# Kernel tuning notes

Measured on AMD Instinct MI355X. Metric: run time of the kernel, lower is better.

## Reference

```python
import jax, jax.numpy as jnp
import numpy as np

D_MODEL = 512
N_HEADS = 8
HEAD_SIZE = 64


def setup_inputs() -> dict:
    key = jax.random.key(0)
    ks = jax.random.split(key, 6)
    B, T = 4, 2048
    x_q = jax.random.normal(ks[0], (B, T, D_MODEL), dtype=jnp.float32)
    s = 1.0 / np.sqrt(D_MODEL)
    # per-head q/k/v projection weights, stacked: [H, head_size, d_model]
    Wq = jax.random.normal(ks[1], (N_HEADS, HEAD_SIZE, D_MODEL), dtype=jnp.float32) * s
    Wk = jax.random.normal(ks[2], (N_HEADS, HEAD_SIZE, D_MODEL), dtype=jnp.float32) * s
    Wv = jax.random.normal(ks[3], (N_HEADS, HEAD_SIZE, D_MODEL), dtype=jnp.float32) * s
    Wp = jax.random.normal(ks[4], (D_MODEL, D_MODEL), dtype=jnp.float32) * s
    bp = jax.random.normal(ks[5], (D_MODEL,), dtype=jnp.float32) * 0.01
    return {"x_q": x_q, "Wq": Wq, "Wk": Wk, "Wv": Wv, "Wp": Wp, "bp": bp}


def reference(x_q, Wq, Wk, Wv, Wp, bp):
    B, T, C = x_q.shape  # C == d_model
    # per-head projections: [B, H, T, K]
    q = jnp.einsum('btd,hkd->bhtk', x_q, Wq)
    k = jnp.einsum('btd,hkd->bhtk', x_q, Wk)
    v = jnp.einsum('btd,hkd->bhtk', x_q, Wv)
    # NOTE: original scales by C**-0.5 with C = d_model (not head_size)
    scores = jnp.einsum('bhtk,bhsk->bhts', q, k) * (C ** -0.5)
    causal = jnp.tril(jnp.ones((T, T), dtype=bool))
    scores = jnp.where(causal, scores, -jnp.inf)
    wei = jax.nn.softmax(scores, axis=-1)  # dropout is identity in eval
    out = jnp.einsum('bhts,bhsk->bhtk', wei, v)
    # concat heads: [B, T, H*K] == [B, T, d_model]
    out = out.transpose(0, 2, 1, 3).reshape(B, T, C)
    return out @ Wp.T + bp
```

## Files before the change

kernel.cpp:

```cpp
#include <hip/hip_runtime.h>
#include <hip/hip_bf16.h>

using bf16x8 = __attribute__((ext_vector_type(8))) __bf16;
using f32x4  = __attribute__((ext_vector_type(4))) float;
using f32x16 = __attribute__((ext_vector_type(16))) float;
using i32x4  = __attribute__((ext_vector_type(4))) int;

#define MFMA_16x16x32(a, b, c) __builtin_amdgcn_mfma_f32_16x16x32_bf16((a), (b), (c), 0, 0, 0)
#define MFMA32(a, b, c)        __builtin_amdgcn_mfma_f32_32x32x16_bf16((a), (b), (c), 0, 0, 0)

__device__ __forceinline__ ushort f2bf(float f) {
    return __builtin_bit_cast(ushort, (__bf16)f);
}
__device__ __forceinline__ unsigned pk_bf16(float lo, float hi) {
    unsigned r;
    asm volatile("v_cvt_pk_bf16_f32 %0, %1, %2" : "=v"(r) : "v"(lo), "v"(hi));
    return r;
}
__device__ __forceinline__ void pl32_swap(unsigned &a, unsigned &b) {
    asm volatile("v_permlane32_swap_b32 %0, %1" : "+v"(a), "+v"(b));
}

__global__ __launch_bounds__(256) void cvt_bf16(
    const float* __restrict__ in, ushort* __restrict__ out, int n)
{
    const int i = (blockIdx.x * 256 + threadIdx.x) * 8;
    if (i + 8 <= n) {
        const f32x4 a = *(const f32x4*)(in + i);
        const f32x4 b = *(const f32x4*)(in + i + 4);
        union { ushort u[8]; i32x4 w; } p;
        #pragma unroll
        for (int j = 0; j < 4; ++j) { p.u[j] = f2bf(a[j]); p.u[4 + j] = f2bf(b[j]); }
        *(i32x4*)(out + i) = p.w;
    }
}

__global__ __launch_bounds__(256) void cvt_w3(
    const float* __restrict__ w0, const float* __restrict__ w1,
    const float* __restrict__ w2, ushort* __restrict__ out)
{
    const int i = (blockIdx.x * 256 + threadIdx.x) * 8;
    const int w = i >> 18, off = i & 262143;
    const float* src = (w == 0) ? w0 : ((w == 1) ? w1 : w2);
    const f32x4 a = *(const f32x4*)(src + off);
    const f32x4 b = *(const f32x4*)(src + off + 4);
    union { ushort u[8]; i32x4 v; } p;
    #pragma unroll
    for (int j = 0; j < 4; ++j) { p.u[j] = f2bf(a[j]); p.u[4 + j] = f2bf(b[j]); }
    *(i32x4*)(out + i) = p.v;
}

__global__ __launch_bounds__(256) void gemm_qkv3(
    const ushort* __restrict__ A, const ushort* __restrict__ Wbf,
    float qscale, ushort* __restrict__ qb, ushort* __restrict__ kb,
    ushort* __restrict__ vb)
{
    __shared__ ushort lA[128][40];
    __shared__ ushort lB[128][40];
    const int wsel = blockIdx.y >> 2;
    const int n0 = (blockIdx.y & 3) * 128;
    const ushort* W = Wbf + wsel * 262144;
    ushort* out = (wsel == 0) ? qb : ((wsel == 1) ? kb : vb);
    const float scale = (wsel == 0) ? qscale : 1.0f;

    const int m0 = blockIdx.x * 128;
    const int tid  = threadIdx.x;
    const int lane = tid & 63;
    const int wave = tid >> 6;
    const int wr = (wave >> 1) * 64, wc = (wave & 1) * 64;
    const int frow = lane & 15, fk = (lane >> 4) * 8;
    const int sr = tid >> 1, scc = (tid & 1) * 16;

    f32x4 acc[4][4] = {};
    i32x4 va0, va1, vb0, vb1;
    auto load = [&](int k0) {
        const ushort* pa = A + (m0 + sr) * 512 + k0 + scc;
        va0 = *(const i32x4*)(pa);
        va1 = *(const i32x4*)(pa + 8);
        const ushort* pb = W + (n0 + sr) * 512 + k0 + scc;
        vb0 = *(const i32x4*)(pb);
        vb1 = *(const i32x4*)(pb + 8);
    };

    load(0);
    for (int t = 0; t < 16; ++t) {
        __syncthreads();
        *(i32x4*)&lA[sr][scc]     = va0;
        *(i32x4*)&lA[sr][scc + 8] = va1;
        *(i32x4*)&lB[sr][scc]     = vb0;
        *(i32x4*)&lB[sr][scc + 8] = vb1;
        if (t + 1 < 16) load((t + 1) * 32);
        __syncthreads();

        bf16x8 af[4], bg[4];
        #pragma unroll
        for (int m = 0; m < 4; ++m) af[m] = *(const bf16x8*)&lA[wr + m * 16 + frow][fk];
        #pragma unroll
        for (int n = 0; n < 4; ++n) bg[n] = *(const bf16x8*)&lB[wc + n * 16 + frow][fk];
        #pragma unroll
        for (int m = 0; m < 4; ++m)
            #pragma unroll
            for (int n = 0; n < 4; ++n)
                acc[m][n] = MFMA_16x16x32(af[m], bg[n], acc[m][n]);
    }

    const int rbase = (lane >> 4) * 4;
    const int ccol  = lane & 15;
    if (wsel == 2) {
        #pragma unroll
        for (int m = 0; m < 4; ++m)
            #pragma unroll
            for (int n = 0; n < 4; ++n) {
                const int col = n0 + wc + n * 16 + ccol;
                const int row0 = m0 + wr + m * 16 + rbase;
                unsigned long long u = 0;
                #pragma unroll
                for (int r = 0; r < 4; ++r)
                    u |= ((unsigned long long)f2bf(acc[m][n][r])) << (16 * r);
                const size_t idx = ((size_t)((row0 >> 11) * 8 + (col >> 6)) * 64
                                    + (col & 63)) * 2048 + (row0 & 2047);
                *(unsigned long long*)(out + idx) = u;
            }
    } else {
        #pragma unroll
        for (int m = 0; m < 4; ++m)
            #pragma unroll
            for (int n = 0; n < 4; ++n) {
                const int col = n0 + wc + n * 16 + ccol;
                #pragma unroll
                for (int r = 0; r < 4; ++r) {
                    const int row = m0 + wr + m * 16 + rbase + r;
                    out[(((row >> 11) * 8 + (col >> 6)) * 2048 + (row & 2047)) * 64 + (col & 63)]
                        = f2bf(acc[m][n][r] * scale);
                }
            }
    }
}

__global__ __launch_bounds__(256) void gemm_out(
    const ushort* __restrict__ A, const float* __restrict__ W,
    const float* __restrict__ bias, float* __restrict__ out)
{
    __shared__ ushort lA[128][40];
    __shared__ ushort lB[128][40];
    const int m0 = blockIdx.x * 128;
    const int n0 = blockIdx.y * 128;
    const int tid  = threadIdx.x;
    const int lane = tid & 63;
    const int wave = tid >> 6;
    const int wr = (wave >> 1) * 64, wc = (wave & 1) * 64;
    const int frow = lane & 15, fk = (lane >> 4) * 8;
    const int sr = tid >> 1, scc = (tid & 1) * 16;

    f32x4 acc[4][4] = {};
    i32x4 va0, va1;
    f32x4 b0, b1, b2, b3;
    auto load = [&](int k0) {
        const int row = m0 + sr, c = k0 + scc;
        const ushort* pa = A + ((((row >> 11) * 8 + (c >> 6)) * 2048 + (row & 2047)) * 64 + (c & 63));
        va0 = *(const i32x4*)(pa);
        va1 = *(const i32x4*)(pa + 8);
        const float* pb = W + (n0 + sr) * 512 + k0 + scc;
        b0 = *(const f32x4*)(pb);
        b1 = *(const f32x4*)(pb + 4);
        b2 = *(const f32x4*)(pb + 8);
        b3 = *(const f32x4*)(pb + 12);
    };

    load(0);
    for (int t = 0; t < 16; ++t) {
        union { ushort u[16]; i32x4 w[2]; } pB;
        #pragma unroll
        for (int j = 0; j < 4; ++j) {
            pB.u[j]      = f2bf(b0[j]);  pB.u[4 + j]  = f2bf(b1[j]);
            pB.u[8 + j]  = f2bf(b2[j]);  pB.u[12 + j] = f2bf(b3[j]);
        }
        __syncthreads();
        *(i32x4*)&lA[sr][scc]     = va0;
        *(i32x4*)&lA[sr][scc + 8] = va1;
        *(i32x4*)&lB[sr][scc]     = pB.w[0];
        *(i32x4*)&lB[sr][scc + 8] = pB.w[1];
        if (t + 1 < 16) load((t + 1) * 32);
        __syncthreads();

        bf16x8 af[4], bg[4];
        #pragma unroll
        for (int m = 0; m < 4; ++m) af[m] = *(const bf16x8*)&lA[wr + m * 16 + frow][fk];
        #pragma unroll
        for (int n = 0; n < 4; ++n) bg[n] = *(const bf16x8*)&lB[wc + n * 16 + frow][fk];
        #pragma unroll
        for (int m = 0; m < 4; ++m)
            #pragma unroll
            for (int n = 0; n < 4; ++n)
                acc[m][n] = MFMA_16x16x32(af[m], bg[n], acc[m][n]);
    }

    const int rbase = (lane >> 4) * 4;
    const int ccol  = lane & 15;
    #pragma unroll
    for (int m = 0; m < 4; ++m)
        #pragma unroll
        for (int n = 0; n < 4; ++n) {
            const int col = n0 + wc + n * 16 + ccol;
            const float bv = bias[col];
            #pragma unroll
            for (int r = 0; r < 4; ++r) {
                const int row = m0 + wr + m * 16 + rbase + r;
                out[row * 512 + col] = acc[m][n][r] + bv;
            }
        }
}

__global__ __launch_bounds__(256, 2) void attn_kernel(
    const ushort* __restrict__ q, const ushort* __restrict__ k,
    const ushort* __restrict__ vt, ushort* __restrict__ att)
{
    __shared__ ushort lK[2][64][64];
    __shared__ ushort lV[2][64][64];

    const int NB   = (int)(gridDim.x * gridDim.y);
    const int NH   = NB >> 4;
    const int half = NB >> 1;
    const int n    = (int)(blockIdx.y * gridDim.x + blockIdx.x);
    const int r    = (n < half) ? n : (NB - 1 - (n - half));
    const int qt0  = (15 - r / NH) * 128;
    const int bh   = r % NH;

    const ushort* Q  = q  + (size_t)bh * 2048 * 64;
    const ushort* K  = k  + (size_t)bh * 2048 * 64;
    const ushort* VT = vt + (size_t)bh * 2048 * 64;
    ushort* O = att + (size_t)bh * 2048 * 64;

    const int tid = threadIdx.x;
    const int wv  = tid >> 6;
    const int l   = tid & 63;
    const int ql  = l & 31;
    const int hi  = l >> 5;
    const int wrow0 = qt0 + wv * 32;
    const int qrow  = wrow0 + ql;
    const int wmax  = wrow0 + 31;
    const int qkey  = ql & 7;
    const float LOG2E = 1.44269504088896f;

    const int srow = tid >> 2;
    const int sg   = (tid & 3) * 2;
    const int skey = srow & 7;

    bf16x8 aq[4];
    #pragma unroll
    for (int kk = 0; kk < 4; ++kk)
        aq[kk] = *(const bf16x8*)(Q + (size_t)qrow * 64 + kk * 16 + hi * 8);

    f32x16 o0 = {}, o1 = {};
    float mrun = -30000.0f, lrun = 0.0f;
    const int nt = qt0 / 64 + 2;

    i32x4 kr0, kr1, vr0, vr1;
    auto loadG = [&](int s0) {
        const ushort* kp = K + (size_t)(s0 + srow) * 64 + (tid & 3) * 16;
        kr0 = *(const i32x4*)(kp);
        kr1 = *(const i32x4*)(kp + 8);
        const ushort* vp = VT + (size_t)srow * 2048 + s0 + (tid & 3) * 16;
        vr0 = *(const i32x4*)(vp);
        vr1 = *(const i32x4*)(vp + 8);
    };
    auto writeL = [&](int b) {
        *(i32x4*)&lK[b][srow][((sg    ) ^ skey) * 8] = kr0;
        *(i32x4*)&lK[b][srow][((sg + 1) ^ skey) * 8] = kr1;
        *(i32x4*)&lV[b][srow][((sg    ) ^ skey) * 8] = vr0;
        *(i32x4*)&lV[b][srow][((sg + 1) ^ skey) * 8] = vr1;
    };

    loadG(0);
    writeL(0);
    if (nt > 1) loadG(64);

    for (int t = 0; t < nt; ++t) {
        const int p  = t & 1;
        const int s0 = t * 64;
        __syncthreads();
        if (t + 1 < nt) writeL(p ^ 1);
        if (t + 2 < nt) loadG(s0 + 128);

        if (s0 > wmax) continue;

        f32x16 sa = {}, sb = {};
        #pragma unroll
        for (int kk = 0; kk < 4; ++kk) {
            const bf16x8 kb0 = *(const bf16x8*)&lK[p][ql]     [((2 * kk + hi) ^ qkey) * 8];
            const bf16x8 kb1 = *(const bf16x8*)&lK[p][32 + ql][((2 * kk + hi) ^ qkey) * 8];
            sa = MFMA32(kb0, aq[kk], sa);
            sb = MFMA32(kb1, aq[kk], sb);
        }

        if (s0 + 63 > wrow0) {
            #pragma unroll
            for (int rr = 0; rr < 16; ++rr) {
                const int cr = (rr & 3) + 8 * (rr >> 2) + 4 * hi;
                if (s0 + cr > qrow)      sa[rr] = -30000.0f;
                if (s0 + 32 + cr > qrow) sb[rr] = -30000.0f;
            }
        }

        float pmax = sa[0];
        #pragma unroll
        for (int rr = 1; rr < 16; ++rr) pmax = fmaxf(pmax, sa[rr]);
        #pragma unroll
        for (int rr = 0; rr < 16; ++rr) pmax = fmaxf(pmax, sb[rr]);
        pmax = fmaxf(pmax, __shfl_xor(pmax, 32));

        if (__any(pmax > mrun + 8.0f)) {
            const float mnew  = fmaxf(mrun, pmax);
            const float alpha = exp2f((mrun - mnew) * LOG2E);
            mrun = mnew;
            lrun *= alpha;
            #pragma unroll
            for (int rr = 0; rr < 16; ++rr) {
                const float ar = __shfl(alpha, (rr & 3) + 8 * (rr >> 2) + 4 * hi);
                o0[rr] *= ar; o1[rr] *= ar;
            }
        }

        const float mb = mrun * LOG2E;
        float ps = 0.0f;
        #pragma unroll
        for (int rr = 0; rr < 16; ++rr) {
            sa[rr] = exp2f(fmaf(sa[rr], LOG2E, -mb));
            sb[rr] = exp2f(fmaf(sb[rr], LOG2E, -mb));
            ps += sa[rr] + sb[rr];
        }
        ps += __shfl_xor(ps, 32);
        lrun += ps;

        unsigned paw[4][4];
        #pragma unroll
        for (int ks = 0; ks < 4; ++ks) {
            const int e = 2 * ks, f = 2 * ks + 1;
            const int ra = 4 * (e & 3), rb = 4 * (f & 3);
            unsigned A0, A1, B0, B1;
            if (e >> 2) { A0 = pk_bf16(sb[ra], sb[ra + 1]); A1 = pk_bf16(sb[ra + 2], sb[ra + 3]); }
            else        { A0 = pk_bf16(sa[ra], sa[ra + 1]); A1 = pk_bf16(sa[ra + 2], sa[ra + 3]); }
            if (f >> 2) { B0 = pk_bf16(sb[rb], sb[rb + 1]); B1 = pk_bf16(sb[rb + 2], sb[rb + 3]); }
            else        { B0 = pk_bf16(sa[rb], sa[rb + 1]); B1 = pk_bf16(sa[rb + 2], sa[rb + 3]); }
            pl32_swap(A0, B0);
            pl32_swap(A1, B1);
            paw[ks][0] = A0; paw[ks][1] = A1; paw[ks][2] = B0; paw[ks][3] = B1;
        }

        #pragma unroll
        for (int ks = 0; ks < 4; ++ks) {
            union { unsigned w[4]; bf16x8 v; } u;
            u.w[0] = paw[ks][0]; u.w[1] = paw[ks][1];
            u.w[2] = paw[ks][2]; u.w[3] = paw[ks][3];
            const bf16x8 v0 = *(const bf16x8*)&lV[p][ql]     [((2 * ks + hi) ^ qkey) * 8];
            const bf16x8 v1 = *(const bf16x8*)&lV[p][32 + ql][((2 * ks + hi) ^ qkey) * 8];
            o0 = MFMA32(u.v, v0, o0);
            o1 = MFMA32(u.v, v1, o1);
        }
    }

    const float linv = 1.0f / fmaxf(lrun, 1e-30f);
    #pragma unroll
    for (int rr = 0; rr < 16; ++rr) {
        const int cr = (rr & 3) + 8 * (rr >> 2) + 4 * hi;
        const float li = __shfl(linv, cr);
        const int row = wrow0 + cr;
        O[(size_t)row * 64 + ql]      = f2bf(o0[rr] * li);
        O[(size_t)row * 64 + 32 + ql] = f2bf(o1[rr] * li);
    }
}

extern "C" void kernel_launch(void* const* d_in, const int* in_sizes, int n_in,
                              void* d_out, int out_size, void* d_ws, size_t ws_size,
                              hipStream_t stream) {
    const float* x  = (const float*)d_in[0];
    const float* Wq = (const float*)d_in[1];
    const float* Wk = (const float*)d_in[2];
    const float* Wv = (const float*)d_in[3];
    const float* Wp = (const float*)d_in[4];
    const float* bp = (const float*)d_in[5];
    float* out = (float*)d_out;

    const size_t NEL  = 4u * 8u * 2048u * 64u;
    const size_t NELB = 8u * 2048u * 64u;
    const float qscale = 0.04419417382415922f;

    if (ws_size >= 3u * NEL * sizeof(ushort)) {
        ushort* xbf = (ushort*)d_out;
        ushort* qb  = xbf + NEL;
        ushort* kb  = (ushort*)d_ws;
        ushort* vb  = kb + NEL;
        ushort* ab  = vb + NEL;
        ushort* wbf = ab;
        hipLaunchKernelGGL(cvt_bf16, dim3((int)(NEL / (256 * 8))), dim3(256), 0, stream,
                           x, xbf, (int)NEL);
        hipLaunchKernelGGL(cvt_w3, dim3(384), dim3(256), 0, stream, Wq, Wk, Wv, wbf);
        hipLaunchKernelGGL(gemm_qkv3, dim3(64, 12), dim3(256), 0, stream,
                           xbf, wbf, qscale, qb, kb, vb);
        hipLaunchKernelGGL(attn_kernel, dim3(16, 32), dim3(256), 0, stream, qb, kb, vb, ab);
        hipLaunchKernelGGL(gemm_out, dim3(64, 4), dim3(256), 0, stream, ab, Wp, bp, out);
    } else {
        ushort* kb = (ushort*)d_ws;
        ushort* vb = kb + NELB;
        ushort* ab = vb + NELB;
        ushort* wbf = ab;
        for (int b = 0; b < 4; ++b) {
            const float* xb = x + (size_t)b * 2048u * 512u;
            float* ob = out + (size_t)b * 2048u * 512u;
            ushort* xbf = (ushort*)ob;
            ushort* qb  = xbf + NELB;
            hipLaunchKernelGGL(cvt_bf16, dim3((int)(NELB / (256 * 8))), dim3(256), 0, stream,
                               xb, xbf, (int)NELB);
            hipLaunchKernelGGL(cvt_w3, dim3(384), dim3(256), 0, stream, Wq, Wk, Wv, wbf);
            hipLaunchKernelGGL(gemm_qkv3, dim3(16, 12), dim3(256), 0, stream,
                               xbf, wbf, qscale, qb, kb, vb);
            hipLaunchKernelGGL(attn_kernel, dim3(16, 8), dim3(256), 0, stream, qb, kb, vb, ab);
            hipLaunchKernelGGL(gemm_out, dim3(16, 4), dim3(256), 0, stream, ab, Wp, bp, ob);
        }
    }
}
```

Baseline: 106.5 us.

## Split attention KV loop across wave pairs with LDS merge of partial softmax

The attention block grows from 4 to 8 waves. Each pair of waves shares the same 32 query rows, and each wave processes alternate 64-key tiles. The pair also splits the K/V global-to-LDS staging between them. At the end, the odd wave writes its partial output and running max/sum to LDS, and the even wave rescales and merges them before writing. The aim is more parallelism per query tile on the long causal loops, in exchange for an extra barrier, the merge traffic, and dropping the explicit two-blocks-per-CU occupancy hint.

```diff
diff --git a/kernel.cpp b/kernel.cpp
--- a/kernel.cpp
+++ b/kernel.cpp
@@ -211,12 +211,12 @@
         }
 }
 
-__global__ __launch_bounds__(256, 2) void attn_kernel(
+__global__ __launch_bounds__(512) void attn_kernel(
     const ushort* __restrict__ q, const ushort* __restrict__ k,
     const ushort* __restrict__ vt, ushort* __restrict__ att)
 {
-    __shared__ ushort lK[2][64][64];
-    __shared__ ushort lV[2][64][64];
+    __shared__ ushort lds[2][2][64][64];
+    __shared__ float  mml[4][2][64];
 
     const int NB   = (int)(gridDim.x * gridDim.y);
     const int NH   = NB >> 4;
@@ -233,17 +233,20 @@
 
     const int tid = threadIdx.x;
     const int wv  = tid >> 6;
+    const int g   = wv >> 1;
+    const int h   = wv & 1;
     const int l   = tid & 63;
     const int ql  = l & 31;
     const int hi  = l >> 5;
-    const int wrow0 = qt0 + wv * 32;
+    const int wrow0 = qt0 + g * 32;
     const int qrow  = wrow0 + ql;
     const int wmax  = wrow0 + 31;
     const int qkey  = ql & 7;
     const float LOG2E = 1.44269504088896f;
 
-    const int srow = tid >> 2;
-    const int sg   = (tid & 3) * 2;
+    const int pid  = g * 64 + l;
+    const int srow = pid >> 2;
+    const int sg   = (pid & 3) * 2;
     const int skey = srow & 7;
 
     bf16x8 aq[4];
@@ -255,20 +258,16 @@
     float mrun = -30000.0f, lrun = 0.0f;
     const int nt = qt0 / 64 + 2;
 
-    i32x4 kr0, kr1, vr0, vr1;
+    i32x4 sr0, sr1;
     auto loadG = [&](int s0) {
-        const ushort* kp = K + (size_t)(s0 + srow) * 64 + (tid & 3) * 16;
-        kr0 = *(const i32x4*)(kp);
-        kr1 = *(const i32x4*)(kp + 8);
-        const ushort* vp = VT + (size_t)srow * 2048 + s0 + (tid & 3) * 16;
-        vr0 = *(const i32x4*)(vp);
-        vr1 = *(const i32x4*)(vp + 8);
+        const ushort* p = h ? (VT + (size_t)srow * 2048 + s0 + sg * 8)
+                            : (K + (size_t)(s0 + srow) * 64 + sg * 8);
+        sr0 = *(const i32x4*)(p);
+        sr1 = *(const i32x4*)(p + 8);
     };
     auto writeL = [&](int b) {
-        *(i32x4*)&lK[b][srow][((sg    ) ^ skey) * 8] = kr0;
-        *(i32x4*)&lK[b][srow][((sg + 1) ^ skey) * 8] = kr1;
-        *(i32x4*)&lV[b][srow][((sg    ) ^ skey) * 8] = vr0;
-        *(i32x4*)&lV[b][srow][((sg + 1) ^ skey) * 8] = vr1;
+        *(i32x4*)&lds[h][b][srow][((sg    ) ^ skey) * 8] = sr0;
+        *(i32x4*)&lds[h][b][srow][((sg + 1) ^ skey) * 8] = sr1;
     };
 
     loadG(0);
@@ -282,13 +281,13 @@
         if (t + 1 < nt) writeL(p ^ 1);
         if (t + 2 < nt) loadG(s0 + 128);
 
-        if (s0 > wmax) continue;
+        if (((t ^ h) & 1) || s0 > wmax) continue;
 
         f32x16 sa = {}, sb = {};
         #pragma unroll
         for (int kk = 0; kk < 4; ++kk) {
-            const bf16x8 kb0 = *(const bf16x8*)&lK[p][ql]     [((2 * kk + hi) ^ qkey) * 8];
-            const bf16x8 kb1 = *(const bf16x8*)&lK[p][32 + ql][((2 * kk + hi) ^ qkey) * 8];
+            const bf16x8 kb0 = *(const bf16x8*)&lds[0][p][ql]     [((2 * kk + hi) ^ qkey) * 8];
+            const bf16x8 kb1 = *(const bf16x8*)&lds[0][p][32 + ql][((2 * kk + hi) ^ qkey) * 8];
             sa = MFMA32(kb0, aq[kk], sa);
             sb = MFMA32(kb1, aq[kk], sb);
         }
@@ -352,21 +351,47 @@
             union { unsigned w[4]; bf16x8 v; } u;
             u.w[0] = paw[ks][0]; u.w[1] = paw[ks][1];
             u.w[2] = paw[ks][2]; u.w[3] = paw[ks][3];
-            const bf16x8 v0 = *(const bf16x8*)&lV[p][ql]     [((2 * ks + hi) ^ qkey) * 8];
-            const bf16x8 v1 = *(const bf16x8*)&lV[p][32 + ql][((2 * ks + hi) ^ qkey) * 8];
+            const bf16x8 v0 = *(const bf16x8*)&lds[1][p][ql]     [((2 * ks + hi) ^ qkey) * 8];
+            const bf16x8 v1 = *(const bf16x8*)&lds[1][p][32 + ql][((2 * ks + hi) ^ qkey) * 8];
             o0 = MFMA32(u.v, v0, o0);
             o1 = MFMA32(u.v, v1, o1);
         }
     }
 
-    const float linv = 1.0f / fmaxf(lrun, 1e-30f);
-    #pragma unroll
-    for (int rr = 0; rr < 16; ++rr) {
-        const int cr = (rr & 3) + 8 * (rr >> 2) + 4 * hi;
-        const float li = __shfl(linv, cr);
-        const int row = wrow0 + cr;
-        O[(size_t)row * 64 + ql]      = f2bf(o0[rr] * li);
-        O[(size_t)row * 64 + 32 + ql] = f2bf(o1[rr] * li);
+    __syncthreads();
+    float* mo = (float*)lds;
+    if (h == 1) {
+        float* base = mo + g * 2048 + l * 32;
+        #pragma unroll
+        for (int rr = 0; rr < 16; ++rr) {
+            base[(rr + l) & 31]      = o0[rr];
+            base[(16 + rr + l) & 31] = o1[rr];
+        }
+        mml[g][0][l] = mrun;
+        mml[g][1][l] = lrun;
+    }
+    __syncthreads();
+    if (h == 0) {
+        const float m1 = mml[g][0][l];
+        const float l1 = mml[g][1][l];
+        const float mm = fmaxf(mrun, m1);
+        const float a0 = exp2f((mrun - mm) * LOG2E);
+        const float a1 = exp2f((m1 - mm) * LOG2E);
+        const float lm   = lrun * a0 + l1 * a1;
+        const float linv = 1.0f / fmaxf(lm, 1e-30f);
+        const float* base = mo + g * 2048 + l * 32;
+        #pragma unroll
+        for (int rr = 0; rr < 16; ++rr) {
+            const int cr = (rr & 3) + 8 * (rr >> 2) + 4 * hi;
+            const float a0r = __shfl(a0, cr);
+            const float a1r = __shfl(a1, cr);
+            const float lir = __shfl(linv, cr);
+            const float po0 = base[(rr + l) & 31];
+            const float po1 = base[(16 + rr + l) & 31];
+            const int row = wrow0 + cr;
+            O[(size_t)row * 64 + ql]      = f2bf((o0[rr] * a0r + po0 * a1r) * lir);
+            O[(size_t)row * 64 + 32 + ql] = f2bf((o1[rr] * a0r + po1 * a1r) * lir);
+        }
     }
 }
 
@@ -397,7 +422,7 @@
         hipLaunchKernelGGL(cvt_w3, dim3(384), dim3(256), 0, stream, Wq, Wk, Wv, wbf);
         hipLaunchKernelGGL(gemm_qkv3, dim3(64, 12), dim3(256), 0, stream,
                            xbf, wbf, qscale, qb, kb, vb);
-        hipLaunchKernelGGL(attn_kernel, dim3(16, 32), dim3(256), 0, stream, qb, kb, vb, ab);
+        hipLaunchKernelGGL(attn_kernel, dim3(16, 32), dim3(512), 0, stream, qb, kb, vb, ab);
         hipLaunchKernelGGL(gemm_out, dim3(64, 4), dim3(256), 0, stream, ab, Wp, bp, out);
     } else {
         ushort* kb = (ushort*)d_ws;
@@ -414,7 +439,7 @@
             hipLaunchKernelGGL(cvt_w3, dim3(384), dim3(256), 0, stream, Wq, Wk, Wv, wbf);
             hipLaunchKernelGGL(gemm_qkv3, dim3(16, 12), dim3(256), 0, stream,
                                xbf, wbf, qscale, qb, kb, vb);
-            hipLaunchKernelGGL(attn_kernel, dim3(16, 8), dim3(256), 0, stream, qb, kb, vb, ab);
+            hipLaunchKernelGGL(attn_kernel, dim3(16, 8), dim3(512), 0, stream, qb, kb, vb, ab);
             hipLaunchKernelGGL(gemm_out, dim3(16, 4), dim3(256), 0, stream, ab, Wp, bp, ob);
         }
     }
```

Measured after the change: 138.4 us. +29.9%, slower.

## Double-buffer QKV GEMM via direct global-to-LDS loads and tree-reduce softmax stats

Applied to the files above, without the earlier changes.

The QKV projection GEMM now stages tiles straight from global memory into double-buffered, XOR-swizzled LDS using global_load_lds. This removes the register round-trip and one barrier per k-step, so the next tile's load can overlap the current MFMAs. Separately, the attention kernel's row max and row sum become tree reductions instead of serial chains, which shortens the dependency latency. The single remaining barrier relies on the async LDS writes having completed, and the swizzle must match between the writers and the readers.

```diff
diff --git a/kernel.cpp b/kernel.cpp
--- a/kernel.cpp
+++ b/kernel.cpp
@@ -8,6 +8,11 @@
 
 #define MFMA_16x16x32(a, b, c) __builtin_amdgcn_mfma_f32_16x16x32_bf16((a), (b), (c), 0, 0, 0)
 #define MFMA32(a, b, c)        __builtin_amdgcn_mfma_f32_32x32x16_bf16((a), (b), (c), 0, 0, 0)
+
+#define GLOAD16(g, l)                                                         \
+    __builtin_amdgcn_global_load_lds(                                         \
+        (const __attribute__((address_space(1))) unsigned int*)(g),           \
+        (__attribute__((address_space(3))) unsigned int*)(l), 16, 0, 0)
 
 __device__ __forceinline__ ushort f2bf(float f) {
     return __builtin_bit_cast(ushort, (__bf16)f);
@@ -55,8 +60,8 @@
     float qscale, ushort* __restrict__ qb, ushort* __restrict__ kb,
     ushort* __restrict__ vb)
 {
-    __shared__ ushort lA[128][40];
-    __shared__ ushort lB[128][40];
+    __shared__ ushort lA[2][128][32];
+    __shared__ ushort lB[2][128][32];
     const int wsel = blockIdx.y >> 2;
     const int n0 = (blockIdx.y & 3) * 128;
     const ushort* W = Wbf + wsel * 262144;
@@ -68,35 +73,33 @@
     const int lane = tid & 63;
     const int wave = tid >> 6;
     const int wr = (wave >> 1) * 64, wc = (wave & 1) * 64;
-    const int frow = lane & 15, fk = (lane >> 4) * 8;
-    const int sr = tid >> 1, scc = (tid & 1) * 16;
+    const int frow = lane & 15;
+    const int fkp  = (((lane >> 4) ^ ((lane >> 1) & 3))) * 8;
+
+    const int srw  = lane >> 2;
+    const int scol = ((lane & 3) ^ ((lane >> 3) & 3)) * 8;
 
     f32x4 acc[4][4] = {};
-    i32x4 va0, va1, vb0, vb1;
-    auto load = [&](int k0) {
-        const ushort* pa = A + (m0 + sr) * 512 + k0 + scc;
-        va0 = *(const i32x4*)(pa);
-        va1 = *(const i32x4*)(pa + 8);
-        const ushort* pb = W + (n0 + sr) * 512 + k0 + scc;
-        vb0 = *(const i32x4*)(pb);
-        vb1 = *(const i32x4*)(pb + 8);
+    auto stage = [&](int k0, int b) {
+        #pragma unroll
+        for (int i = 0; i < 2; ++i) {
+            const int rb = (wave * 2 + i) * 16;
+            GLOAD16(A + (size_t)(m0 + rb + srw) * 512 + k0 + scol, &lA[b][rb][0]);
+            GLOAD16(W + (size_t)(n0 + rb + srw) * 512 + k0 + scol, &lB[b][rb][0]);
+        }
     };
 
-    load(0);
+    stage(0, 0);
     for (int t = 0; t < 16; ++t) {
+        const int p = t & 1;
         __syncthreads();
-        *(i32x4*)&lA[sr][scc]     = va0;
-        *(i32x4*)&lA[sr][scc + 8] = va1;
-        *(i32x4*)&lB[sr][scc]     = vb0;
-        *(i32x4*)&lB[sr][scc + 8] = vb1;
-        if (t + 1 < 16) load((t + 1) * 32);
-        __syncthreads();
+        if (t + 1 < 16) stage((t + 1) * 32, p ^ 1);
 
         bf16x8 af[4], bg[4];
         #pragma unroll
-        for (int m = 0; m < 4; ++m) af[m] = *(const bf16x8*)&lA[wr + m * 16 + frow][fk];
-        #pragma unroll
-        for (int n = 0; n < 4; ++n) bg[n] = *(const bf16x8*)&lB[wc + n * 16 + frow][fk];
+        for (int m = 0; m < 4; ++m) af[m] = *(const bf16x8*)&lA[p][wr + m * 16 + frow][fkp];
+        #pragma unroll
+        for (int n = 0; n < 4; ++n) bg[n] = *(const bf16x8*)&lB[p][wc + n * 16 + frow][fkp];
         #pragma unroll
         for (int m = 0; m < 4; ++m)
             #pragma unroll
@@ -302,12 +305,14 @@
             }
         }
 
-        float pmax = sa[0];
-        #pragma unroll
-        for (int rr = 1; rr < 16; ++rr) pmax = fmaxf(pmax, sa[rr]);
-        #pragma unroll
-        for (int rr = 0; rr < 16; ++rr) pmax = fmaxf(pmax, sb[rr]);
-        pmax = fmaxf(pmax, __shfl_xor(pmax, 32));
+        float tm[16];
+        #pragma unroll
+        for (int rr = 0; rr < 16; ++rr) tm[rr] = fmaxf(sa[rr], sb[rr]);
+        #pragma unroll
+        for (int s = 8; s > 0; s >>= 1)
+            #pragma unroll
+            for (int rr = 0; rr < s; ++rr) tm[rr] = fmaxf(tm[rr], tm[rr + s]);
+        float pmax = fmaxf(tm[0], __shfl_xor(tm[0], 32));
 
         if (__any(pmax > mrun + 8.0f)) {
             const float mnew  = fmaxf(mrun, pmax);
@@ -322,15 +327,19 @@
         }
 
         const float mb = mrun * LOG2E;
-        float ps = 0.0f;
         #pragma unroll
         for (int rr = 0; rr < 16; ++rr) {
             sa[rr] = exp2f(fmaf(sa[rr], LOG2E, -mb));
             sb[rr] = exp2f(fmaf(sb[rr], LOG2E, -mb));
-            ps += sa[rr] + sb[rr];
-        }
-        ps += __shfl_xor(ps, 32);
-        lrun += ps;
+        }
+        float tu[16];
+        #pragma unroll
+        for (int rr = 0; rr < 16; ++rr) tu[rr] = sa[rr] + sb[rr];
+        #pragma unroll
+        for (int s = 8; s > 0; s >>= 1)
+            #pragma unroll
+            for (int rr = 0; rr < s; ++rr) tu[rr] += tu[rr + s];
+        lrun += tu[0] + __shfl_xor(tu[0], 32);
 
         unsigned paw[4][4];
         #pragma unroll
```

After: 104.1 us. -2.2%, faster.
